# Kernel tuning notes

Measured on AMD Instinct MI355X. Metric: run time of the kernel, lower is better.

The kernel has to match this reference:

```python
import jax, jax.numpy as jnp
import numpy as np

TEMPERATURE = 8.0  # sqrt(head_dim=64)


def setup_inputs() -> dict:
    key = jax.random.key(0)
    kq, kk, kv, km = jax.random.split(key, 4)
    B, S, D = 16, 2048, 64
    q = jax.random.normal(kq, (B, S, D), dtype=jnp.float32)
    k = jax.random.normal(kk, (B, S, D), dtype=jnp.float32)
    v = jax.random.normal(kv, (B, S, D), dtype=jnp.float32)
    mask = jax.random.randint(km, (B, S, S), 0, 2).astype(jnp.bool_)
    return {"q": q, "k": k, "v": v, "mask": mask}


def reference(q, k, v, mask):
    # latent = q @ k^T / temperature  -> [B, Sq, Sk]
    latent = jnp.einsum('bqd,bkd->bqk', q, k) / TEMPERATURE
    # NOTE: the original fills masked positions with 1e-9 (NOT -inf); keep faithful.
    latent = jnp.where(mask, jnp.float32(1e-9), latent)
    attn = jax.nn.softmax(latent, axis=-1)
    return jnp.einsum('bqk,bkd->bqd', attn, v)
```

## Files before the change

kernel.cpp:

```cpp
#include <hip/hip_runtime.h>
#include <hip/hip_bf16.h>

#define BB 16
#define SS 2048
#define DD 64
#define NT_TILES (SS / 128)
#define TILE_BYTES 16384

typedef __attribute__((ext_vector_type(8)))  unsigned short ushort8;
typedef __attribute__((ext_vector_type(8)))  __bf16 bf16x8;
typedef __attribute__((ext_vector_type(16))) float f32x16;
typedef __attribute__((ext_vector_type(4)))  unsigned int uint4v;

static __device__ __forceinline__ unsigned short f2bf(float x) {
    return __builtin_bit_cast(unsigned short, __float2bfloat16(x));
}
static __device__ __forceinline__ unsigned pk2(float a, float b) {
    return (unsigned)f2bf(a) | ((unsigned)f2bf(b) << 16);
}
union F4 { float4 v; float a[4]; };

#define GLDS16(src, dst) __builtin_amdgcn_global_load_lds(                 \
    (const __attribute__((address_space(1))) unsigned int*)(src),          \
    (__attribute__((address_space(3))) unsigned int*)(dst), 16, 0, 0)

__global__ __launch_bounds__(256)
void prepack_kernel(const float* __restrict__ K, const float* __restrict__ V,
                    char* __restrict__ wsK, char* __restrict__ wsV) {
    __shared__ __align__(16) char smem[32768];
    char* Ks = smem;
    char* Vs = smem + 16384;
    const int t  = threadIdx.x;
    const int kt = blockIdx.x;
    const int b  = blockIdx.y;
    const float* Kg = K + (size_t)b * SS * DD;
    const float* Vg = V + (size_t)b * SS * DD;

    #pragma unroll
    for (int j = 0; j < 4; j++) {
        const int idx = 2 * t + 512 * j;
        const int row = idx >> 4;
        const int g   = (idx & 15) >> 1;
        const float* src = Kg + (size_t)(kt * 128) * DD + (size_t)idx * 4;
        F4 fa, fb; fa.v = *(const float4*)src; fb.v = *(const float4*)(src + 4);
        ushort8 u;
        #pragma unroll
        for (int e = 0; e < 4; e++) { u[e] = f2bf(fa.a[e]); u[e + 4] = f2bf(fb.a[e]); }
        *(ushort8*)(Ks + row * 128 + ((g ^ (row & 7)) * 16)) = u;
    }
    {
        const int d0v = (t & 15) * 4;
        const int kkb = (t >> 4) * 4;
        #pragma unroll
        for (int it2 = 0; it2 < 2; it2++) {
            const int kk = kkb + 64 * it2;
            const float* src = Vg + (size_t)(kt * 128 + kk) * DD + d0v;
            F4 r0, r1, r2, r3;
            r0.v = *(const float4*)(src);
            r1.v = *(const float4*)(src + DD);
            r2.v = *(const float4*)(src + 2 * DD);
            r3.v = *(const float4*)(src + 3 * DD);
            #pragma unroll
            for (int e = 0; e < 4; e++) {
                const int d = d0v + e;
                const uint2 wv = make_uint2(pk2(r0.a[e], r1.a[e]), pk2(r2.a[e], r3.a[e]));
                *(uint2*)(Vs + d * 256 + (((kk >> 3) ^ (d & 15)) * 16) + (kk & 7) * 2) = wv;
            }
        }
    }
    __syncthreads();
    char* dK = wsK + (size_t)(b * NT_TILES + kt) * TILE_BYTES;
    char* dV = wsV + (size_t)(b * NT_TILES + kt) * TILE_BYTES;
    #pragma unroll
    for (int j = 0; j < 4; j++) {
        *(float4*)(dK + t * 16 + j * 4096) = *(const float4*)(Ks + t * 16 + j * 4096);
        *(float4*)(dV + t * 16 + j * 4096) = *(const float4*)(Vs + t * 16 + j * 4096);
    }
}

__global__ __launch_bounds__(256, 4)
void sdpa_mfma_kernel(const float* __restrict__ Q, const char* __restrict__ wsK,
                      const char* __restrict__ wsV, const unsigned int* __restrict__ M,
                      float* __restrict__ O) {
    __shared__ __align__(16) char smem[37120];
    char* Ks = smem;
    char* Vs = smem + 16384;
    char* Ms = smem + 32768;
    char* Qs = smem + 32768;
    float* red  = (float*)smem;
    float* denx = (float*)(smem + 32768);

    const int t    = threadIdx.x;
    const int lane = t & 63;
    const int l31  = lane & 31;
    const int half = lane >> 5;
    const int kh   = t >> 6;
    const int b    = blockIdx.y;
    const int q0   = blockIdx.x * 32;

    const unsigned int* Mg = M + (size_t)b * SS * SS + (size_t)q0 * SS;

    {
        const int sr = t >> 3, sc = t & 7;
        const float* src = Q + ((size_t)b * SS + q0 + sr) * DD + sc * 8;
        F4 f0, f1; f0.v = *(const float4*)src; f1.v = *(const float4*)(src + 4);
        ushort8 u;
        #pragma unroll
        for (int e = 0; e < 4; e++) {
            u[e]     = f2bf(f0.a[e] * 0.125f);
            u[e + 4] = f2bf(f1.a[e] * 0.125f);
        }
        *(ushort8*)(Qs + sr * 128 + ((sc ^ (sr & 7)) * 16)) = u;
    }
    __syncthreads();

    const int qrow = l31;
    bf16x8 bq[4];
    #pragma unroll
    for (int dc = 0; dc < 4; dc++)
        bq[dc] = __builtin_bit_cast(bf16x8, *(const ushort8*)(
            Qs + qrow * 128 + (((2 * dc + half) ^ (qrow & 7)) * 16)));
    __syncthreads();

    f32x16 On0, On1;
    #pragma unroll
    for (int i = 0; i < 16; i++) { On0[i] = 0.f; On1[i] = 0.f; }
    float den_acc = 0.f;

    const int krow = 32 * kh + l31;

    for (int kt = 0; kt < NT_TILES; ++kt) {
        const char* tK = wsK + (size_t)(b * NT_TILES + kt) * TILE_BYTES;
        const char* tV = wsV + (size_t)(b * NT_TILES + kt) * TILE_BYTES;
        #pragma unroll
        for (int j = 0; j < 4; j++) {
            GLDS16(tK + t * 16 + j * 4096, Ks + kh * 1024 + j * 4096);
            GLDS16(tV + t * 16 + j * 4096, Vs + kh * 1024 + j * 4096);
        }
        {
            const int sr = t >> 3, sc = t & 7;
            const unsigned int* Mw = Mg + (size_t)sr * SS + kt * 128 + sc * 16;
            unsigned wd[4];
            #pragma unroll
            for (int g = 0; g < 4; g++) {
                const uint4v u = __builtin_nontemporal_load((const uint4v*)(Mw + 4 * g));
                wd[g] = (u[0] ? 1u : 0u) | (u[1] ? 0x100u : 0u) |
                        (u[2] ? 0x10000u : 0u) | (u[3] ? 0x1000000u : 0u);
            }
            *(uint2*)(Ms + sr * 136 + sc * 16)     = make_uint2(wd[0], wd[1]);
            *(uint2*)(Ms + sr * 136 + sc * 16 + 8) = make_uint2(wd[2], wd[3]);
        }
        __syncthreads();

        f32x16 S;
        #pragma unroll
        for (int i = 0; i < 16; i++) S[i] = 0.f;
        #pragma unroll
        for (int dc = 0; dc < 4; dc++) {
            bf16x8 ak = __builtin_bit_cast(bf16x8, *(const ushort8*)(
                Ks + krow * 128 + (((2 * dc + half) ^ (krow & 7)) * 16)));
            S = __builtin_amdgcn_mfma_f32_32x32x16_bf16(ak, bq[dc], S, 0, 0, 0);
        }

        float p[16];
        #pragma unroll
        for (int g = 0; g < 4; g++) {
            const unsigned mw = *(const unsigned*)(Ms + qrow * 136 + 32 * kh + 8 * g + 4 * half);
            #pragma unroll
            for (int e = 0; e < 4; e++) {
                const float ev = __expf(S[4 * g + e]);
                const float pv = ((mw >> (8 * e)) & 0xffu) ? 1.0f : ev;
                p[4 * g + e] = pv;
                den_acc += pv;
            }
        }

        #pragma unroll
        for (int s2 = 0; s2 < 2; s2++) {
            const unsigned o0 = pk2(p[8 * s2 + 0], p[8 * s2 + 1]);
            const unsigned o1 = pk2(p[8 * s2 + 2], p[8 * s2 + 3]);
            const unsigned o2 = pk2(p[8 * s2 + 4], p[8 * s2 + 5]);
            const unsigned o3 = pk2(p[8 * s2 + 6], p[8 * s2 + 7]);
            const unsigned s0 = half ? o0 : o2;
            const unsigned s1 = half ? o1 : o3;
            const unsigned r0 = (unsigned)__shfl_xor((int)s0, 32, 64);
            const unsigned r1 = (unsigned)__shfl_xor((int)s1, 32, 64);
            uint4 bu;
            bu.x = half ? r0 : o0;
            bu.y = half ? r1 : o1;
            bu.z = half ? o2 : r0;
            bu.w = half ? o3 : r1;
            const bf16x8 bp = __builtin_bit_cast(bf16x8, bu);
            #pragma unroll
            for (int dc = 0; dc < 2; dc++) {
                const int vrow = 32 * dc + l31;
                bf16x8 av = __builtin_bit_cast(bf16x8, *(const ushort8*)(
                    Vs + vrow * 256 + (((4 * kh + 2 * s2 + half) ^ (vrow & 15)) * 16)));
                if (dc == 0) On0 = __builtin_amdgcn_mfma_f32_32x32x16_bf16(av, bp, On0, 0, 0, 0);
                else         On1 = __builtin_amdgcn_mfma_f32_32x32x16_bf16(av, bp, On1, 0, 0, 0);
            }
        }
        __syncthreads();
    }

    const float den_tot = den_acc + __shfl_xor(den_acc, 32, 64);

    __syncthreads();
    if (kh != 0) {
        #pragma unroll
        for (int dc = 0; dc < 2; dc++)
            #pragma unroll
            for (int g = 0; g < 4; g++) {
                const f32x16& Oc = dc ? On1 : On0;
                float4 st;
                st.x = Oc[4 * g + 0]; st.y = Oc[4 * g + 1];
                st.z = Oc[4 * g + 2]; st.w = Oc[4 * g + 3];
                *(float4*)((char*)red + (kh - 1) * 8192 + (dc * 4 + g) * 1024 + lane * 16) = st;
            }
        if (lane < 32) denx[kh * 32 + l31] = den_tot;
    }
    __syncthreads();
    if (kh == 0) {
        const float inv = 1.0f / (den_tot + denx[32 + l31] + denx[64 + l31] + denx[96 + l31]);
        float* Og = O + ((size_t)b * SS + q0 + qrow) * DD;
        #pragma unroll
        for (int dc = 0; dc < 2; dc++)
            #pragma unroll
            for (int g = 0; g < 4; g++) {
                const f32x16& Oc = dc ? On1 : On0;
                float4 st;
                st.x = Oc[4 * g + 0]; st.y = Oc[4 * g + 1];
                st.z = Oc[4 * g + 2]; st.w = Oc[4 * g + 3];
                #pragma unroll
                for (int w2 = 0; w2 < 3; w2++) {
                    const float4 pr = *(const float4*)((char*)red + w2 * 8192 +
                                                       (dc * 4 + g) * 1024 + lane * 16);
                    st.x += pr.x; st.y += pr.y; st.z += pr.z; st.w += pr.w;
                }
                st.x *= inv; st.y *= inv; st.z *= inv; st.w *= inv;
                *(float4*)(Og + 32 * dc + 8 * g + 4 * half) = st;
            }
    }
}

extern "C" void kernel_launch(void* const* d_in, const int* in_sizes, int n_in,
                              void* d_out, int out_size, void* d_ws, size_t ws_size,
                              hipStream_t stream) {
    const float* q = (const float*)d_in[0];
    const float* k = (const float*)d_in[1];
    const float* v = (const float*)d_in[2];
    const unsigned int* m = (const unsigned int*)d_in[3];
    float* out = (float*)d_out;

    char* wsK = (char*)d_ws;
    char* wsV = (char*)d_ws + (size_t)BB * NT_TILES * TILE_BYTES;

    dim3 pgrid(NT_TILES, BB);
    prepack_kernel<<<pgrid, 256, 0, stream>>>(k, v, wsK, wsV);

    dim3 grid(SS / 32, BB);
    sdpa_mfma_kernel<<<grid, 256, 0, stream>>>(q, wsK, wsV, m, out);
}
```

Before: 412.6 us.

## Load K/V/mask fragments directly from global into registers, dropping LDS staging

```diff
diff --git a/kernel.cpp b/kernel.cpp
--- a/kernel.cpp
+++ b/kernel.cpp
@@ -19,10 +19,6 @@
     return (unsigned)f2bf(a) | ((unsigned)f2bf(b) << 16);
 }
 union F4 { float4 v; float a[4]; };
-
-#define GLDS16(src, dst) __builtin_amdgcn_global_load_lds(                 \
-    (const __attribute__((address_space(1))) unsigned int*)(src),          \
-    (__attribute__((address_space(3))) unsigned int*)(dst), 16, 0, 0)
 
 __global__ __launch_bounds__(256)
 void prepack_kernel(const float* __restrict__ K, const float* __restrict__ V,
@@ -82,13 +78,10 @@
 void sdpa_mfma_kernel(const float* __restrict__ Q, const char* __restrict__ wsK,
                       const char* __restrict__ wsV, const unsigned int* __restrict__ M,
                       float* __restrict__ O) {
-    __shared__ __align__(16) char smem[37120];
-    char* Ks = smem;
-    char* Vs = smem + 16384;
-    char* Ms = smem + 32768;
-    char* Qs = smem + 32768;
+    __shared__ __align__(16) char smem[25088];
+    char* Qs = smem;
     float* red  = (float*)smem;
-    float* denx = (float*)(smem + 32768);
+    float* denx = (float*)(smem + 24576);
 
     const int t    = threadIdx.x;
     const int lane = t & 63;
@@ -98,8 +91,6 @@
     const int b    = blockIdx.y;
     const int q0   = blockIdx.x * 32;
 
-    const unsigned int* Mg = M + (size_t)b * SS * SS + (size_t)q0 * SS;
-
     {
         const int sr = t >> 3, sc = t & 7;
         const float* src = Q + ((size_t)b * SS + q0 + sr) * DD + sc * 8;
@@ -120,7 +111,6 @@
     for (int dc = 0; dc < 4; dc++)
         bq[dc] = __builtin_bit_cast(bf16x8, *(const ushort8*)(
             Qs + qrow * 128 + (((2 * dc + half) ^ (qrow & 7)) * 16)));
-    __syncthreads();
 
     f32x16 On0, On1;
     #pragma unroll
@@ -128,48 +118,48 @@
     float den_acc = 0.f;
 
     const int krow = 32 * kh + l31;
+    const char* tKbase = wsK + (size_t)b * NT_TILES * TILE_BYTES;
+    const char* tVbase = wsV + (size_t)b * NT_TILES * TILE_BYTES;
+    const unsigned int* Mrow = M + (size_t)b * SS * SS + (size_t)(q0 + qrow) * SS
+                                 + 32 * kh + 4 * half;
 
     for (int kt = 0; kt < NT_TILES; ++kt) {
-        const char* tK = wsK + (size_t)(b * NT_TILES + kt) * TILE_BYTES;
-        const char* tV = wsV + (size_t)(b * NT_TILES + kt) * TILE_BYTES;
-        #pragma unroll
-        for (int j = 0; j < 4; j++) {
-            GLDS16(tK + t * 16 + j * 4096, Ks + kh * 1024 + j * 4096);
-            GLDS16(tV + t * 16 + j * 4096, Vs + kh * 1024 + j * 4096);
-        }
-        {
-            const int sr = t >> 3, sc = t & 7;
-            const unsigned int* Mw = Mg + (size_t)sr * SS + kt * 128 + sc * 16;
-            unsigned wd[4];
-            #pragma unroll
-            for (int g = 0; g < 4; g++) {
-                const uint4v u = __builtin_nontemporal_load((const uint4v*)(Mw + 4 * g));
-                wd[g] = (u[0] ? 1u : 0u) | (u[1] ? 0x100u : 0u) |
-                        (u[2] ? 0x10000u : 0u) | (u[3] ? 0x1000000u : 0u);
-            }
-            *(uint2*)(Ms + sr * 136 + sc * 16)     = make_uint2(wd[0], wd[1]);
-            *(uint2*)(Ms + sr * 136 + sc * 16 + 8) = make_uint2(wd[2], wd[3]);
-        }
-        __syncthreads();
+        const char* tK = tKbase + (size_t)kt * TILE_BYTES;
+        const char* tV = tVbase + (size_t)kt * TILE_BYTES;
+
+        bf16x8 ak[4];
+        #pragma unroll
+        for (int dc = 0; dc < 4; dc++)
+            ak[dc] = __builtin_bit_cast(bf16x8, *(const ushort8*)(
+                tK + krow * 128 + (((2 * dc + half) ^ (krow & 7)) * 16)));
+        uint4v mw[4];
+        #pragma unroll
+        for (int g = 0; g < 4; g++)
+            mw[g] = __builtin_nontemporal_load((const uint4v*)(Mrow + kt * 128 + 8 * g));
+        bf16x8 av[2][2];
+        #pragma unroll
+        for (int s2 = 0; s2 < 2; s2++)
+            #pragma unroll
+            for (int dc = 0; dc < 2; dc++) {
+                const int vrow = 32 * dc + l31;
+                av[s2][dc] = __builtin_bit_cast(bf16x8, *(const ushort8*)(
+                    tV + vrow * 256 + (((4 * kh + 2 * s2 + half) ^ (vrow & 15)) * 16)));
+            }
 
         f32x16 S;
         #pragma unroll
         for (int i = 0; i < 16; i++) S[i] = 0.f;
         #pragma unroll
-        for (int dc = 0; dc < 4; dc++) {
-            bf16x8 ak = __builtin_bit_cast(bf16x8, *(const ushort8*)(
-                Ks + krow * 128 + (((2 * dc + half) ^ (krow & 7)) * 16)));
-            S = __builtin_amdgcn_mfma_f32_32x32x16_bf16(ak, bq[dc], S, 0, 0, 0);
-        }
+        for (int dc = 0; dc < 4; dc++)
+            S = __builtin_amdgcn_mfma_f32_32x32x16_bf16(ak[dc], bq[dc], S, 0, 0, 0);
 
         float p[16];
         #pragma unroll
         for (int g = 0; g < 4; g++) {
-            const unsigned mw = *(const unsigned*)(Ms + qrow * 136 + 32 * kh + 8 * g + 4 * half);
             #pragma unroll
             for (int e = 0; e < 4; e++) {
                 const float ev = __expf(S[4 * g + e]);
-                const float pv = ((mw >> (8 * e)) & 0xffu) ? 1.0f : ev;
+                const float pv = mw[g][e] ? 1.0f : ev;
                 p[4 * g + e] = pv;
                 den_acc += pv;
             }
@@ -193,14 +183,10 @@
             const bf16x8 bp = __builtin_bit_cast(bf16x8, bu);
             #pragma unroll
             for (int dc = 0; dc < 2; dc++) {
-                const int vrow = 32 * dc + l31;
-                bf16x8 av = __builtin_bit_cast(bf16x8, *(const ushort8*)(
-                    Vs + vrow * 256 + (((4 * kh + 2 * s2 + half) ^ (vrow & 15)) * 16)));
-                if (dc == 0) On0 = __builtin_amdgcn_mfma_f32_32x32x16_bf16(av, bp, On0, 0, 0, 0);
-                else         On1 = __builtin_amdgcn_mfma_f32_32x32x16_bf16(av, bp, On1, 0, 0, 0);
-            }
-        }
-        __syncthreads();
+                if (dc == 0) On0 = __builtin_amdgcn_mfma_f32_32x32x16_bf16(av[s2][0], bp, On0, 0, 0, 0);
+                else         On1 = __builtin_amdgcn_mfma_f32_32x32x16_bf16(av[s2][1], bp, On1, 0, 0, 0);
+            }
+        }
     }
 
     const float den_tot = den_acc + __shfl_xor(den_acc, 32, 64);
```

Measured after the change: 510.6 us. 1.24x slower.
